# Optimization experiments

Measured on AMD Instinct MI355X. Metric: run time of the kernel, lower is better.

Reference implementation:

```python
import jax, jax.numpy as jnp
import numpy as np

B, S, D = 2, 2048, 1024
H = 16
HD = D // H
WINDOW = 128
SCALE = HD ** -0.5


def setup_inputs() -> dict:
    key = jax.random.key(0)
    ks = jax.random.split(key, 5)
    x = jax.random.normal(ks[0], (B, S, D), dtype=jnp.float32)
    # nn.Linear(dim, 3*dim) and nn.Linear(dim, dim), stored as [in, out] for x @ W
    w_qkv = jax.random.normal(ks[1], (D, 3 * D), dtype=jnp.float32) * (D ** -0.5)
    b_qkv = jax.random.normal(ks[2], (3 * D,), dtype=jnp.float32) * 0.02
    w_out = jax.random.normal(ks[3], (D, D), dtype=jnp.float32) * (D ** -0.5)
    b_out = jax.random.normal(ks[4], (D,), dtype=jnp.float32) * 0.02
    return {"x": x, "w_qkv": w_qkv, "b_qkv": b_qkv, "w_out": w_out, "b_out": b_out}


def _local_mask(seq_len):
    idx = jnp.arange(seq_len)
    band = jnp.abs(idx[:, None] - idx[None, :]) <= WINDOW // 2
    return jnp.where(band, 0.0, -jnp.inf).astype(jnp.float32)  # [S, S]


def reference(x, w_qkv, b_qkv, w_out, b_out):
    b, s, _ = x.shape
    qkv = x @ w_qkv + b_qkv                       # [B, S, 3D]
    qkv = qkv.reshape(b, s, 3, H, HD).transpose(2, 0, 3, 1, 4)  # [3, B, H, S, HD]
    q, k, v = qkv[0], qkv[1], qkv[2]
    mask = _local_mask(s)                          # [S, S]
    scores = jnp.einsum("bhqd,bhkd->bhqk", q, k) * SCALE + mask
    attn = jax.nn.softmax(scores, axis=-1)         # dropout is identity at eval
    out = jnp.einsum("bhqk,bhkd->bhqd", attn, v)   # [B, H, S, HD]
    out = out.transpose(0, 2, 1, 3).reshape(b, s, D)
    return out @ w_out + b_out
```

## Files before the change

### kernel.cpp

```cpp
#include <hip/hip_runtime.h>
#include <hip/hip_bf16.h>

typedef short bf16x8 __attribute__((ext_vector_type(8)));
typedef float f32x4 __attribute__((ext_vector_type(4)));
typedef unsigned short ushort_t;

#define SQ 2048
#define DIM 1024
#define NH 16
#define HD 64

__device__ __forceinline__ ushort_t f2bf(float f) {
    __hip_bfloat16 h = __float2bfloat16(f);
    return *reinterpret_cast<ushort_t*>(&h);
}

__device__ __forceinline__ void load_lds16(const void* g, void* l) {
    __builtin_amdgcn_global_load_lds(
        (const __attribute__((address_space(1))) unsigned int*)g,
        (__attribute__((address_space(3))) unsigned int*)l, 16, 0, 0);
}

__global__ void prep_kernel(const float* __restrict__ x, ushort_t* __restrict__ xb,
                            const float* __restrict__ w_qkv, ushort_t* __restrict__ wqkvT,
                            const float* __restrict__ w_out, ushort_t* __restrict__ woutT) {
    __shared__ ushort_t tile[32][33];
    const int bid = blockIdx.x;
    const int tid = threadIdx.x;
    if (bid < 1024) {
        int i = bid * 256 + tid;
        const int stride = 1024 * 256;
        const int n4 = 4096 * 1024 / 4;
        for (; i < n4; i += stride) {
            float4 f = reinterpret_cast<const float4*>(x)[i];
            ushort4 o;
            o.x = f2bf(f.x); o.y = f2bf(f.y); o.z = f2bf(f.z); o.w = f2bf(f.w);
            reinterpret_cast<ushort4*>(xb)[i] = o;
        }
        return;
    }
    if (bid < 4096) {
        int idx = bid - 1024;
        int cx = idx % 96, ry = idx / 96;
        int c0 = cx * 32, r0 = ry * 32;
        int tx = tid & 31, ty = tid >> 5;
#pragma unroll
        for (int i = 0; i < 32; i += 8)
            tile[ty + i][tx] = f2bf(w_qkv[(size_t)(r0 + ty + i) * 3072 + c0 + tx]);
        __syncthreads();
#pragma unroll
        for (int i = 0; i < 32; i += 8)
            wqkvT[(size_t)(c0 + ty + i) * 1024 + r0 + tx] = tile[tx][ty + i];
        return;
    }
    {
        int idx = bid - 4096;
        int cx = idx % 32, ry = idx / 32;
        int c0 = cx * 32, r0 = ry * 32;
        int tx = tid & 31, ty = tid >> 5;
#pragma unroll
        for (int i = 0; i < 32; i += 8)
            tile[ty + i][tx] = f2bf(w_out[(size_t)(r0 + ty + i) * 1024 + c0 + tx]);
        __syncthreads();
#pragma unroll
        for (int i = 0; i < 32; i += 8)
            woutT[(size_t)(c0 + ty + i) * 1024 + r0 + tx] = tile[tx][ty + i];
    }
}

__global__ void transpose_v(const ushort_t* __restrict__ qkv, ushort_t* __restrict__ vt) {
    __shared__ ushort_t tile[32][33];
    int s0 = blockIdx.x * 32, d0 = blockIdx.y * 32;
    int bh = blockIdx.z;
    int b = bh >> 4, h = bh & 15;
    const ushort_t* src = qkv + (size_t)(b * SQ) * 3072 + 2048 + h * 64;
    ushort_t* dst = vt + (size_t)bh * HD * SQ;
    int tx = threadIdx.x, ty = threadIdx.y;
#pragma unroll
    for (int i = 0; i < 32; i += 8)
        tile[ty + i][tx] = src[(size_t)(s0 + ty + i) * 3072 + d0 + tx];
    __syncthreads();
#pragma unroll
    for (int i = 0; i < 32; i += 8)
        dst[(size_t)(d0 + ty + i) * SQ + s0 + tx] = tile[tx][ty + i];
}


#define STAGE_U(Gptr, ldk, grow0, kcol, regionbase)                          \
  { int row_ = tid >> 3;                                                      \
    int sc_ = (tid & 7) ^ (row_ & 7);                                         \
    load_lds16((Gptr) + (size_t)((grow0) + row_) * (ldk) + (kcol) + sc_ * 8,  \
               (regionbase) + tid * 16); }

#define DS_A192(BASE, EXTRA)                                                  \
  _Pragma("unroll") for (int kk_ = 0; kk_ < 2; ++kk_)                         \
  _Pragma("unroll") for (int m_ = 0; m_ < 4; ++m_)                            \
    a[kk_][m_] = *reinterpret_cast<const bf16x8*>((BASE) + (EXTRA) + offA[kk_][m_]);

#define DS_B192(BASE)                                                         \
  _Pragma("unroll") for (int kk_ = 0; kk_ < 2; ++kk_)                         \
  _Pragma("unroll") for (int n_ = 0; n_ < 3; ++n_)                            \
    b[kk_][n_] = *reinterpret_cast<const bf16x8*>((BASE) + offB[kk_][n_]);

#define BAR_LGKM                                                              \
  __builtin_amdgcn_s_barrier();                                               \
  asm volatile("s_waitcnt lgkmcnt(0)" ::: "memory");                          \
  __builtin_amdgcn_sched_barrier(0);

#define MFMA_Q(MQ)                                                            \
  __builtin_amdgcn_s_setprio(1);                                              \
  _Pragma("unroll") for (int kk_ = 0; kk_ < 2; ++kk_)                         \
  _Pragma("unroll") for (int m_ = 0; m_ < 4; ++m_)                            \
  _Pragma("unroll") for (int n_ = 0; n_ < 3; ++n_)                            \
    acc[(MQ)*4 + m_][n_] = __builtin_amdgcn_mfma_f32_16x16x32_bf16(           \
        a[kk_][m_], b[kk_][n_], acc[(MQ)*4 + m_][n_], 0, 0, 0);               \
  __builtin_amdgcn_s_setprio(0);

__global__ __launch_bounds__(512, 2)
void gemm192_bt(const ushort_t* __restrict__ A, const ushort_t* __restrict__ Bt,
                const float* __restrict__ bias, ushort_t* __restrict__ Cout,
                int M, int N, int K, int nbn) {
    __shared__ char sm[114688];
    const int tid = threadIdx.x;
    const int lane = tid & 63;
    const int w = tid >> 6;
    const int wm = w >> 2, wn = w & 3;
    const int r = lane & 15, hi = lane >> 4;

    const int cpx = gridDim.x >> 3;
    const int bid = blockIdx.x;
    const int x = (bid & 7) * cpx + (bid >> 3);
    const int bm = x / nbn, bn = x % nbn;
    const int m0 = bm * 256, n0 = bn * 192;

    const int NT = K >> 6;
    const int NI = NT >> 1;

    char* const A0 = sm;
    char* const B0 = sm + 32768;
    char* const A1 = sm + 57344;
    char* const B1 = sm + 90112;

    int offA[2][4], offB[2][3];
#pragma unroll
    for (int kk = 0; kk < 2; ++kk) {
#pragma unroll
        for (int m = 0; m < 4; ++m) {
            int rowL = wm * 128 + m * 16 + r;
            offA[kk][m] = rowL * 128 + (((kk * 4 + hi) ^ (rowL & 7)) * 16);
        }
#pragma unroll
        for (int n = 0; n < 3; ++n) {
            int rowL = wn * 48 + n * 16 + r;
            offB[kk][n] = rowL * 128 + (((kk * 4 + hi) ^ (rowL & 7)) * 16);
        }
    }

    f32x4 acc[8][3];
#pragma unroll
    for (int am = 0; am < 8; ++am)
#pragma unroll
        for (int an = 0; an < 3; ++an) acc[am][an] = (f32x4){0.f, 0.f, 0.f, 0.f};

    bf16x8 a[2][4], b[2][3];

    STAGE_U(A,  K, m0,        0, A0);
    STAGE_U(A,  K, m0 + 64,   0, A0 + 8192);
    STAGE_U(A,  K, m0 + 128,  0, A0 + 16384);
    STAGE_U(A,  K, m0 + 192,  0, A0 + 24576);
    STAGE_U(Bt, K, n0,        0, B0);
    STAGE_U(Bt, K, n0 + 64,   0, B0 + 8192);
    STAGE_U(Bt, K, n0 + 128,  0, B0 + 16384);
    STAGE_U(A,  K, m0,       64, A1);
    STAGE_U(A,  K, m0 + 128, 64, A1 + 16384);
    asm volatile("s_waitcnt vmcnt(2)" ::: "memory");
    __builtin_amdgcn_s_barrier();

    for (int i = 0; i < NI; ++i) {
        const int k1 = (2 * i + 1) * 64;
        const int k2 = ((2 * i + 2) % NT) * 64;
        const int k3 = ((2 * i + 3) % NT) * 64;

        STAGE_U(A,  K, m0 + 64,  k1, A1 + 8192);
        STAGE_U(A,  K, m0 + 192, k1, A1 + 24576);
        STAGE_U(Bt, K, n0,       k1, B1);
        STAGE_U(Bt, K, n0 + 64,  k1, B1 + 8192);
        STAGE_U(Bt, K, n0 + 128, k1, B1 + 16384);
        DS_A192(A0, 0); DS_B192(B0);
        BAR_LGKM; MFMA_Q(0);
        __builtin_amdgcn_s_barrier();

        STAGE_U(A, K, m0,       k2, A0);
        STAGE_U(A, K, m0 + 128, k2, A0 + 16384);
        DS_A192(A0, 8192);
        BAR_LGKM; MFMA_Q(1);
        asm volatile("s_waitcnt vmcnt(2)" ::: "memory");
        __builtin_amdgcn_s_barrier();

        STAGE_U(A,  K, m0 + 64,  k2, A0 + 8192);
        STAGE_U(A,  K, m0 + 192, k2, A0 + 24576);
        STAGE_U(Bt, K, n0,       k2, B0);
        STAGE_U(Bt, K, n0 + 64,  k2, B0 + 8192);
        STAGE_U(Bt, K, n0 + 128, k2, B0 + 16384);
        DS_A192(A1, 0); DS_B192(B1);
        BAR_LGKM; MFMA_Q(0);
        __builtin_amdgcn_s_barrier();

        STAGE_U(A, K, m0,       k3, A1);
        STAGE_U(A, K, m0 + 128, k3, A1 + 16384);
        DS_A192(A1, 8192);
        BAR_LGKM; MFMA_Q(1);
        asm volatile("s_waitcnt vmcnt(2)" ::: "memory");
        __builtin_amdgcn_s_barrier();
    }

#pragma unroll
    for (int am = 0; am < 8; ++am) {
        int rowg = m0 + wm * 128 + (am >> 2) * 64 + (am & 3) * 16 + hi * 4;
#pragma unroll
        for (int an = 0; an < 3; ++an) {
            int colg = n0 + wn * 48 + an * 16 + r;
            float bv = bias[colg];
#pragma unroll
            for (int j = 0; j < 4; ++j) {
                float v = acc[am][an][j] + bv;
                Cout[(size_t)(rowg + j) * N + colg] = f2bf(v);
            }
        }
    }
}


#define G2_DSA(BASE, MQ)                                                      \
  _Pragma("unroll") for (int kk_ = 0; kk_ < 2; ++kk_)                         \
  _Pragma("unroll") for (int m_ = 0; m_ < 2; ++m_)                            \
    a2[kk_][m_] = *reinterpret_cast<const bf16x8*>((BASE) + offA2[kk_][(MQ)*2 + m_]);

#define G2_DSB(BASE)                                                          \
  _Pragma("unroll") for (int kk_ = 0; kk_ < 2; ++kk_)                         \
  _Pragma("unroll") for (int n_ = 0; n_ < 2; ++n_)                            \
    b2[kk_][n_] = *reinterpret_cast<const bf16x8*>((BASE) + offB2[kk_][n_]);

#define G2_MFMA(MQ)                                                           \
  __builtin_amdgcn_s_setprio(1);                                              \
  _Pragma("unroll") for (int kk_ = 0; kk_ < 2; ++kk_)                         \
  _Pragma("unroll") for (int m_ = 0; m_ < 2; ++m_)                            \
  _Pragma("unroll") for (int n_ = 0; n_ < 2; ++n_)                            \
    acc[(MQ)*2 + m_][n_] = __builtin_amdgcn_mfma_f32_16x16x32_bf16(           \
        a2[kk_][m_], b2[kk_][n_], acc[(MQ)*2 + m_][n_], 0, 0, 0);             \
  __builtin_amdgcn_s_setprio(0);

__global__ __launch_bounds__(512, 2)
void gemm128_4ph(const ushort_t* __restrict__ A, const ushort_t* __restrict__ Bt,
                 const float* __restrict__ bias, float* __restrict__ Cout,
                 int M, int N, int K, int nbn) {
    __shared__ char sm[65536];
    const int tid = threadIdx.x;
    const int lane = tid & 63;
    const int w = tid >> 6;
    const int wm = w >> 2, wn = w & 3;
    const int r = lane & 15, hi = lane >> 4;

    const int cpx = gridDim.x >> 3;
    const int bid = blockIdx.x;
    const int x = (bid & 7) * cpx + (bid >> 3);
    const int bm = x / nbn, bn = x % nbn;
    const int m0 = bm * 128, n0 = bn * 128;

    const int NT = K >> 6;
    const int NI = NT >> 1;

    char* const A0 = sm;
    char* const B0 = sm + 16384;
    char* const A1 = sm + 32768;
    char* const B1 = sm + 49152;

    int offA2[2][4], offB2[2][2];
#pragma unroll
    for (int kk = 0; kk < 2; ++kk) {
#pragma unroll
        for (int m = 0; m < 4; ++m) {
            int rowL = wm * 64 + m * 16 + r;
            offA2[kk][m] = rowL * 128 + (((kk * 4 + hi) ^ (rowL & 7)) * 16);
        }
#pragma unroll
        for (int n = 0; n < 2; ++n) {
            int rowL = wn * 32 + n * 16 + r;
            offB2[kk][n] = rowL * 128 + (((kk * 4 + hi) ^ (rowL & 7)) * 16);
        }
    }

    f32x4 acc[4][2];
#pragma unroll
    for (int am = 0; am < 4; ++am)
#pragma unroll
        for (int an = 0; an < 2; ++an) acc[am][an] = (f32x4){0.f, 0.f, 0.f, 0.f};

    bf16x8 a2[2][2], b2[2][2];

    STAGE_U(A,  K, m0,       0, A0);
    STAGE_U(A,  K, m0 + 64,  0, A0 + 8192);
    STAGE_U(Bt, K, n0,       0, B0);
    STAGE_U(Bt, K, n0 + 64,  0, B0 + 8192);
    STAGE_U(Bt, K, n0,      64, B1);
    STAGE_U(Bt, K, n0 + 64, 64, B1 + 8192);
    asm volatile("s_waitcnt vmcnt(2)" ::: "memory");
    __builtin_amdgcn_s_barrier();

    for (int i = 0; i < NI; ++i) {
        const int k1 = (2 * i + 1) * 64;
        const int k2 = ((2 * i + 2) % NT) * 64;
        const int k3 = ((2 * i + 3) % NT) * 64;

        STAGE_U(A, K, m0,      k1, A1);
        STAGE_U(A, K, m0 + 64, k1, A1 + 8192);
        G2_DSA(A0, 0); G2_DSB(B0);
        BAR_LGKM; G2_MFMA(0);
        __builtin_amdgcn_s_barrier();

        STAGE_U(Bt, K, n0,      k2, B0);
        STAGE_U(Bt, K, n0 + 64, k2, B0 + 8192);
        G2_DSA(A0, 1);
        BAR_LGKM; G2_MFMA(1);
        asm volatile("s_waitcnt vmcnt(2)" ::: "memory");
        __builtin_amdgcn_s_barrier();

        STAGE_U(A, K, m0,      k2, A0);
        STAGE_U(A, K, m0 + 64, k2, A0 + 8192);
        G2_DSA(A1, 0); G2_DSB(B1);
        BAR_LGKM; G2_MFMA(0);
        __builtin_amdgcn_s_barrier();

        STAGE_U(Bt, K, n0,      k3, B1);
        STAGE_U(Bt, K, n0 + 64, k3, B1 + 8192);
        G2_DSA(A1, 1);
        BAR_LGKM; G2_MFMA(1);
        asm volatile("s_waitcnt vmcnt(2)" ::: "memory");
        __builtin_amdgcn_s_barrier();
    }

#pragma unroll
    for (int am = 0; am < 4; ++am) {
        int rowg = m0 + wm * 64 + am * 16 + hi * 4;
#pragma unroll
        for (int an = 0; an < 2; ++an) {
            int colg = n0 + wn * 32 + an * 16 + r;
            float bv = bias[colg];
#pragma unroll
            for (int j = 0; j < 4; ++j)
                Cout[(size_t)(rowg + j) * N + colg] = acc[am][an][j] + bv;
        }
    }
}

__global__ __launch_bounds__(256, 4)
void attn_kernel(const ushort_t* __restrict__ qkv, const ushort_t* __restrict__ vt,
                 ushort_t* __restrict__ attn_out) {
    __shared__ char smem[25600];

    const int bid0 = blockIdx.x;
    const int bid = (bid0 & 7) * 128 + (bid0 >> 3);
    const int qb = bid & 31;
    const int h = (bid >> 5) & 15;
    const int b = bid >> 9;
    const int q0 = qb * 64;
    const int kstart = (q0 - 64 > 0) ? (q0 - 64) : 0;

    const int tid = threadIdx.x;
    const int lane = tid & 63;
    const int w = tid >> 6;
    const int r = lane & 15, hi = lane >> 4;

#pragma unroll
    for (int i = 0; i < 6; ++i) {
        int task = i * 256 + tid;
        int row = task >> 3, ch = task & 7;
        int key = kstart + row;
        uint4 v = make_uint4(0u, 0u, 0u, 0u);
        if (key < SQ)
            v = *reinterpret_cast<const uint4*>(
                qkv + (size_t)(b * SQ + key) * 3072 + 1024 + h * 64 + ch * 8);
        int byte = row * 128 + ch * 16; byte ^= (row & 7) << 4;
        *reinterpret_cast<uint4*>(smem + byte) = v;
    }

    const ushort_t* qrow = qkv + (size_t)(b * SQ + q0 + w * 16 + r) * 3072 + h * 64;
    bf16x8 aq0 = *reinterpret_cast<const bf16x8*>(qrow + hi * 8);
    bf16x8 aq1 = *reinterpret_cast<const bf16x8*>(qrow + 32 + hi * 8);

    __syncthreads();

    const int delta = q0 - kstart;
    const int base = w * 16 + delta;
    int tmin = (base - 64) >> 4; if (tmin < 0) tmin = 0;
    int tmax = (base + 79) >> 4;
    int tcap = (SQ - 1 - kstart) >> 4; if (tmax > tcap) tmax = tcap;
    if (tmax > 11) tmax = 11;
    const int ksmin = tmin >> 1, ksmax = tmax >> 1;

    f32x4 acc[12];
#pragma unroll
    for (int t = 0; t < 12; ++t) acc[t] = (f32x4){0.f, 0.f, 0.f, 0.f};
#pragma unroll
    for (int t = 0; t < 12; ++t) {
        if (t < tmin || t > tmax) continue;
#pragma unroll
        for (int ks = 0; ks < 2; ++ks) {
            int row = t * 16 + r;
            int byte = row * 128 + ks * 64 + hi * 16; byte ^= (row & 7) << 4;
            bf16x8 bk = *reinterpret_cast<const bf16x8*>(smem + byte);
            acc[t] = __builtin_amdgcn_mfma_f32_16x16x32_bf16(
                ks == 0 ? aq0 : aq1, bk, acc[t], 0, 0, 0);
        }
    }

    float mrow[4], lrow[4];
#pragma unroll
    for (int t = 0; t < 12; ++t) {
        if (t < tmin || t > tmax) continue;
        int key = kstart + t * 16 + r;
#pragma unroll
        for (int j = 0; j < 4; ++j) {
            int qrow_g = q0 + w * 16 + hi * 4 + j;
            int dd = key - qrow_g; if (dd < 0) dd = -dd;
            bool valid = (key < SQ) && (dd <= 64);
            acc[t][j] = valid ? acc[t][j] * 0.125f : -1e30f;
        }
    }
#pragma unroll
    for (int j = 0; j < 4; ++j) {
        float m = -1e30f;
#pragma unroll
        for (int t = 0; t < 12; ++t) {
            if (t < tmin || t > tmax) continue;
            m = fmaxf(m, acc[t][j]);
        }
        m = fmaxf(m, __shfl_xor(m, 1));
        m = fmaxf(m, __shfl_xor(m, 2));
        m = fmaxf(m, __shfl_xor(m, 4));
        m = fmaxf(m, __shfl_xor(m, 8));
        mrow[j] = m;
    }
#pragma unroll
    for (int j = 0; j < 4; ++j) {
        float s = 0.f;
#pragma unroll
        for (int t = 0; t < 12; ++t) {
            if (t < tmin || t > tmax) continue;
            float p = __expf(acc[t][j] - mrow[j]);
            acc[t][j] = p;
            s += p;
        }
        s += __shfl_xor(s, 1);
        s += __shfl_xor(s, 2);
        s += __shfl_xor(s, 4);
        s += __shfl_xor(s, 8);
        lrow[j] = s;
    }

    __syncthreads();

#pragma unroll
    for (int t = 0; t < 12; ++t) {
        int col = t * 16 + r;
        bool inb = (t >= tmin) && (t <= tmax);
#pragma unroll
        for (int j = 0; j < 4; ++j) {
            int rowL = w * 16 + hi * 4 + j;
            ushort_t pv = inb ? f2bf(acc[t][j]) : (ushort_t)0;
            *reinterpret_cast<ushort_t*>(smem + rowL * 400 + col * 2) = pv;
        }
    }

    const ushort_t* vtb = vt + (size_t)(b * NH + h) * HD * SQ;
    f32x4 oacc[4];
#pragma unroll
    for (int dt = 0; dt < 4; ++dt) oacc[dt] = (f32x4){0.f, 0.f, 0.f, 0.f};
#pragma unroll
    for (int ks = 0; ks < 6; ++ks) {
        if (ks < ksmin || ks > ksmax) continue;
        int k0 = ks * 32 + hi * 8;
        bf16x8 ap = *reinterpret_cast<const bf16x8*>(
            smem + (w * 16 + r) * 400 + k0 * 2);
        int k8 = kstart + k0;
        if (k8 > SQ - 8) k8 = SQ - 8;
#pragma unroll
        for (int dt = 0; dt < 4; ++dt) {
            int d = dt * 16 + r;
            bf16x8 bv = *reinterpret_cast<const bf16x8*>(vtb + (size_t)d * SQ + k8);
            oacc[dt] = __builtin_amdgcn_mfma_f32_16x16x32_bf16(ap, bv, oacc[dt], 0, 0, 0);
        }
    }

    float inv[4];
#pragma unroll
    for (int j = 0; j < 4; ++j) inv[j] = 1.0f / lrow[j];
#pragma unroll
    for (int dt = 0; dt < 4; ++dt) {
        int d = dt * 16 + r;
#pragma unroll
        for (int j = 0; j < 4; ++j) {
            int rowL = w * 16 + hi * 4 + j;
            *reinterpret_cast<ushort_t*>(smem + rowL * 400 + d * 2) =
                f2bf(oacc[dt][j] * inv[j]);
        }
    }
    __syncthreads();

#pragma unroll
    for (int it = 0; it < 2; ++it) {
        int task = it * 256 + tid;
        int row = task >> 3, c = task & 7;
        uint4 v = *reinterpret_cast<const uint4*>(smem + row * 400 + c * 16);
        *reinterpret_cast<uint4*>(
            attn_out + (size_t)(b * SQ + q0 + row) * 1024 + h * 64 + c * 8) = v;
    }
}

extern "C" void kernel_launch(void* const* d_in, const int* in_sizes, int n_in,
                              void* d_out, int out_size, void* d_ws, size_t ws_size,
                              hipStream_t stream) {
    const float* x     = (const float*)d_in[0];
    const float* w_qkv = (const float*)d_in[1];
    const float* b_qkv = (const float*)d_in[2];
    const float* w_out = (const float*)d_in[3];
    const float* b_out = (const float*)d_in[4];
    float* out = (float*)d_out;

    char* ws = (char*)d_ws;
    ushort_t* xb    = (ushort_t*)(ws);
    ushort_t* wqkvT = (ushort_t*)(ws + 8388608);
    ushort_t* woutT = (ushort_t*)(ws + 14680064);
    ushort_t* qkv   = (ushort_t*)(ws + 16777216);
    ushort_t* aout  = (ushort_t*)(ws + 41943040);
    ushort_t* vtbuf = (ushort_t*)(ws + 50331648);

    prep_kernel<<<5120, 256, 0, stream>>>(x, xb, w_qkv, wqkvT, w_out, woutT);

    gemm192_bt<<<256, 512, 0, stream>>>(xb, wqkvT, b_qkv, qkv, 4096, 3072, 1024, 16);
    transpose_v<<<dim3(64, 2, 32), dim3(32, 8), 0, stream>>>(qkv, vtbuf);
    attn_kernel<<<1024, 256, 0, stream>>>(qkv, vtbuf, aout);
    gemm128_4ph<<<256, 512, 0, stream>>>(aout, woutT, b_out, out, 4096, 1024, 1024, 8);
}
```

Measured before the change: 79.27 us.

## Use 4-wave 64x64 warp tiles in output GEMM and write attention output directly

The output-projection GEMM moves from 8 waves with 64x32 warp tiles to 4 waves (256 threads) with 64x64 warp tiles. Each wave now issues a 4x4 MFMA grid per k-step, which improves register-level operand reuse and lowers LDS read traffic per MFMA. Staging uses two loads per thread, so the vmcnt waits are adjusted. Separately, the attention kernel drops its LDS round-trip and writes bf16 results straight to global memory with scattered 2-byte stores, trading coalescing for one fewer barrier and less LDS traffic.

```diff
diff --git a/kernel.cpp b/kernel.cpp
--- a/kernel.cpp
+++ b/kernel.cpp
@@ -231,34 +231,41 @@
 }
 
 
-#define G2_DSA(BASE, MQ)                                                      \
+#define STAGE_U2(Gptr, ldk, grow0, kcol, regionbase)                          \
+  { _Pragma("unroll")                                                         \
+    for (int j_ = 0; j_ < 2; ++j_) {                                          \
+      int task_ = j_ * 256 + tid;                                             \
+      int row_ = task_ >> 3;                                                  \
+      int sc_ = (task_ & 7) ^ (row_ & 7);                                     \
+      load_lds16((Gptr) + (size_t)((grow0) + row_) * (ldk) + (kcol) + sc_ * 8,\
+                 (regionbase) + task_ * 16); } }
+
+#define G2_A(BASE, KK)                                                        \
+  _Pragma("unroll") for (int m_ = 0; m_ < 4; ++m_)                            \
+    a2[m_] = *reinterpret_cast<const bf16x8*>((BASE) + offA2[KK][m_]);
+
+#define G2_B(BASE)                                                            \
   _Pragma("unroll") for (int kk_ = 0; kk_ < 2; ++kk_)                         \
-  _Pragma("unroll") for (int m_ = 0; m_ < 2; ++m_)                            \
-    a2[kk_][m_] = *reinterpret_cast<const bf16x8*>((BASE) + offA2[kk_][(MQ)*2 + m_]);
-
-#define G2_DSB(BASE)                                                          \
-  _Pragma("unroll") for (int kk_ = 0; kk_ < 2; ++kk_)                         \
-  _Pragma("unroll") for (int n_ = 0; n_ < 2; ++n_)                            \
+  _Pragma("unroll") for (int n_ = 0; n_ < 4; ++n_)                            \
     b2[kk_][n_] = *reinterpret_cast<const bf16x8*>((BASE) + offB2[kk_][n_]);
 
-#define G2_MFMA(MQ)                                                           \
+#define G2_MFMA(KK)                                                           \
   __builtin_amdgcn_s_setprio(1);                                              \
-  _Pragma("unroll") for (int kk_ = 0; kk_ < 2; ++kk_)                         \
-  _Pragma("unroll") for (int m_ = 0; m_ < 2; ++m_)                            \
-  _Pragma("unroll") for (int n_ = 0; n_ < 2; ++n_)                            \
-    acc[(MQ)*2 + m_][n_] = __builtin_amdgcn_mfma_f32_16x16x32_bf16(           \
-        a2[kk_][m_], b2[kk_][n_], acc[(MQ)*2 + m_][n_], 0, 0, 0);             \
+  _Pragma("unroll") for (int m_ = 0; m_ < 4; ++m_)                            \
+  _Pragma("unroll") for (int n_ = 0; n_ < 4; ++n_)                            \
+    acc[m_][n_] = __builtin_amdgcn_mfma_f32_16x16x32_bf16(                    \
+        a2[m_], b2[KK][n_], acc[m_][n_], 0, 0, 0);                            \
   __builtin_amdgcn_s_setprio(0);
 
-__global__ __launch_bounds__(512, 2)
-void gemm128_4ph(const ushort_t* __restrict__ A, const ushort_t* __restrict__ Bt,
-                 const float* __restrict__ bias, float* __restrict__ Cout,
-                 int M, int N, int K, int nbn) {
+__global__ __launch_bounds__(256, 2)
+void gemm128_v2(const ushort_t* __restrict__ A, const ushort_t* __restrict__ Bt,
+                const float* __restrict__ bias, float* __restrict__ Cout,
+                int M, int N, int K, int nbn) {
     __shared__ char sm[65536];
     const int tid = threadIdx.x;
     const int lane = tid & 63;
     const int w = tid >> 6;
-    const int wm = w >> 2, wn = w & 3;
+    const int wm = w >> 1, wn = w & 1;
     const int r = lane & 15, hi = lane >> 4;
 
     const int cpx = gridDim.x >> 3;
@@ -275,7 +282,7 @@
     char* const A1 = sm + 32768;
     char* const B1 = sm + 49152;
 
-    int offA2[2][4], offB2[2][2];
+    int offA2[2][4], offB2[2][4];
 #pragma unroll
     for (int kk = 0; kk < 2; ++kk) {
 #pragma unroll
@@ -284,27 +291,27 @@
             offA2[kk][m] = rowL * 128 + (((kk * 4 + hi) ^ (rowL & 7)) * 16);
         }
 #pragma unroll
-        for (int n = 0; n < 2; ++n) {
-            int rowL = wn * 32 + n * 16 + r;
+        for (int n = 0; n < 4; ++n) {
+            int rowL = wn * 64 + n * 16 + r;
             offB2[kk][n] = rowL * 128 + (((kk * 4 + hi) ^ (rowL & 7)) * 16);
         }
     }
 
-    f32x4 acc[4][2];
-#pragma unroll
-    for (int am = 0; am < 4; ++am)
-#pragma unroll
-        for (int an = 0; an < 2; ++an) acc[am][an] = (f32x4){0.f, 0.f, 0.f, 0.f};
-
-    bf16x8 a2[2][2], b2[2][2];
-
-    STAGE_U(A,  K, m0,       0, A0);
-    STAGE_U(A,  K, m0 + 64,  0, A0 + 8192);
-    STAGE_U(Bt, K, n0,       0, B0);
-    STAGE_U(Bt, K, n0 + 64,  0, B0 + 8192);
-    STAGE_U(Bt, K, n0,      64, B1);
-    STAGE_U(Bt, K, n0 + 64, 64, B1 + 8192);
-    asm volatile("s_waitcnt vmcnt(2)" ::: "memory");
+    f32x4 acc[4][4];
+#pragma unroll
+    for (int m = 0; m < 4; ++m)
+#pragma unroll
+        for (int n = 0; n < 4; ++n) acc[m][n] = (f32x4){0.f, 0.f, 0.f, 0.f};
+
+    bf16x8 a2[4], b2[2][4];
+
+    STAGE_U2(A,  K, m0,       0, A0);
+    STAGE_U2(A,  K, m0 + 64,  0, A0 + 8192);
+    STAGE_U2(Bt, K, n0,       0, B0);
+    STAGE_U2(Bt, K, n0 + 64,  0, B0 + 8192);
+    STAGE_U2(Bt, K, n0,      64, B1);
+    STAGE_U2(Bt, K, n0 + 64, 64, B1 + 8192);
+    asm volatile("s_waitcnt vmcnt(4)" ::: "memory");
     __builtin_amdgcn_s_barrier();
 
     for (int i = 0; i < NI; ++i) {
@@ -312,43 +319,43 @@
         const int k2 = ((2 * i + 2) % NT) * 64;
         const int k3 = ((2 * i + 3) % NT) * 64;
 
-        STAGE_U(A, K, m0,      k1, A1);
-        STAGE_U(A, K, m0 + 64, k1, A1 + 8192);
-        G2_DSA(A0, 0); G2_DSB(B0);
+        STAGE_U2(A, K, m0,      k1, A1);
+        STAGE_U2(A, K, m0 + 64, k1, A1 + 8192);
+        G2_A(A0, 0); G2_B(B0);
         BAR_LGKM; G2_MFMA(0);
         __builtin_amdgcn_s_barrier();
 
-        STAGE_U(Bt, K, n0,      k2, B0);
-        STAGE_U(Bt, K, n0 + 64, k2, B0 + 8192);
-        G2_DSA(A0, 1);
+        STAGE_U2(Bt, K, n0,      k2, B0);
+        STAGE_U2(Bt, K, n0 + 64, k2, B0 + 8192);
+        G2_A(A0, 1);
         BAR_LGKM; G2_MFMA(1);
-        asm volatile("s_waitcnt vmcnt(2)" ::: "memory");
-        __builtin_amdgcn_s_barrier();
-
-        STAGE_U(A, K, m0,      k2, A0);
-        STAGE_U(A, K, m0 + 64, k2, A0 + 8192);
-        G2_DSA(A1, 0); G2_DSB(B1);
+        asm volatile("s_waitcnt vmcnt(4)" ::: "memory");
+        __builtin_amdgcn_s_barrier();
+
+        STAGE_U2(A, K, m0,      k2, A0);
+        STAGE_U2(A, K, m0 + 64, k2, A0 + 8192);
+        G2_A(A1, 0); G2_B(B1);
         BAR_LGKM; G2_MFMA(0);
         __builtin_amdgcn_s_barrier();
 
-        STAGE_U(Bt, K, n0,      k3, B1);
-        STAGE_U(Bt, K, n0 + 64, k3, B1 + 8192);
-        G2_DSA(A1, 1);
+        STAGE_U2(Bt, K, n0,      k3, B1);
+        STAGE_U2(Bt, K, n0 + 64, k3, B1 + 8192);
+        G2_A(A1, 1);
         BAR_LGKM; G2_MFMA(1);
-        asm volatile("s_waitcnt vmcnt(2)" ::: "memory");
-        __builtin_amdgcn_s_barrier();
-    }
-
-#pragma unroll
-    for (int am = 0; am < 4; ++am) {
-        int rowg = m0 + wm * 64 + am * 16 + hi * 4;
-#pragma unroll
-        for (int an = 0; an < 2; ++an) {
-            int colg = n0 + wn * 32 + an * 16 + r;
+        asm volatile("s_waitcnt vmcnt(4)" ::: "memory");
+        __builtin_amdgcn_s_barrier();
+    }
+
+#pragma unroll
+    for (int m = 0; m < 4; ++m) {
+        int rowg = m0 + wm * 64 + m * 16 + hi * 4;
+#pragma unroll
+        for (int n = 0; n < 4; ++n) {
+            int colg = n0 + wn * 64 + n * 16 + r;
             float bv = bias[colg];
 #pragma unroll
             for (int j = 0; j < 4; ++j)
-                Cout[(size_t)(rowg + j) * N + colg] = acc[am][an][j] + bv;
+                Cout[(size_t)(rowg + j) * N + colg] = acc[m][n][j] + bv;
         }
     }
 }
@@ -500,20 +507,9 @@
         int d = dt * 16 + r;
 #pragma unroll
         for (int j = 0; j < 4; ++j) {
-            int rowL = w * 16 + hi * 4 + j;
-            *reinterpret_cast<ushort_t*>(smem + rowL * 400 + d * 2) =
-                f2bf(oacc[dt][j] * inv[j]);
-        }
-    }
-    __syncthreads();
-
-#pragma unroll
-    for (int it = 0; it < 2; ++it) {
-        int task = it * 256 + tid;
-        int row = task >> 3, c = task & 7;
-        uint4 v = *reinterpret_cast<const uint4*>(smem + row * 400 + c * 16);
-        *reinterpret_cast<uint4*>(
-            attn_out + (size_t)(b * SQ + q0 + row) * 1024 + h * 64 + c * 8) = v;
+            int q = q0 + w * 16 + hi * 4 + j;
+            attn_out[(size_t)(b * SQ + q) * 1024 + h * 64 + d] = f2bf(oacc[dt][j] * inv[j]);
+        }
     }
 }
 
@@ -540,5 +536,5 @@
     gemm192_bt<<<256, 512, 0, stream>>>(xb, wqkvT, b_qkv, qkv, 4096, 3072, 1024, 16);
     transpose_v<<<dim3(64, 2, 32), dim3(32, 8), 0, stream>>>(qkv, vtbuf);
     attn_kernel<<<1024, 256, 0, stream>>>(qkv, vtbuf, aout);
-    gemm128_4ph<<<256, 512, 0, stream>>>(aout, woutT, b_out, out, 4096, 1024, 1024, 8);
-}
+    gemm128_v2<<<256, 256, 0, stream>>>(aout, woutT, b_out, out, 4096, 1024, 1024, 8);
+}
```

New measurement: 80.47 us. No clear change (+1.5%).
